# Performance work log

Measured on AMD Instinct MI355X. Metric: run time of the kernel, lower is better.

## Reference

```python
import jax, jax.numpy as jnp
import numpy as np


def setup_inputs() -> dict:
    key = jax.random.key(0)
    k1, k2 = jax.random.split(key)
    B, N, Fin, Fout, K = 4, 4096, 64, 64, 20
    x = jax.random.normal(k1, (B, N, Fin), dtype=jnp.float32)
    # nn.Linear(2*Fin, Fout): weight [Fout, 2*Fin], bias [Fout]
    W = jax.random.normal(k2, (Fout, 2 * Fin), dtype=jnp.float32) * (1.0 / np.sqrt(2 * Fin))
    b = jnp.zeros((Fout,), dtype=jnp.float32)
    return {"x": x, "W": W, "b": b, "k": K}


def _edge_features(x, k):
    # x: [B, N, F] -> edge features [B, N, k, 2F]
    # pairwise squared distance: ||xi||^2 - 2 xi.xj + ||xj||^2
    xs = jnp.sum(x * x, axis=2, keepdims=True)            # [B, N, 1]
    dist = xs - 2.0 * jnp.einsum('bnf,bmf->bnm', x, x) + jnp.swapaxes(xs, 1, 2)  # [B, N, N]
    idx = jnp.argsort(dist, axis=2)[:, :, 1:k + 1]        # skip self -> [B, N, k]
    # gather neighbor features per batch (vectorized index_select)
    neighbors = jax.vmap(lambda xb, ib: xb[ib])(x, idx)   # [B, N, k, F]
    central = jnp.broadcast_to(x[:, :, None, :], neighbors.shape)
    return jnp.concatenate([central, neighbors - central], axis=3)  # [B, N, k, 2F]


def reference(x, W, b, k):
    ee = _edge_features(x, k)                 # [B, N, k, 2F]
    h = jnp.einsum('bnkc,oc->bnko', ee, W) + b  # Linear(2F -> Fout)
    return jnp.max(h, axis=2)                 # max over k neighbors -> [B, N, Fout]
```

## Files before the change

kernel.cpp:

```cpp
#include <hip/hip_runtime.h>
#include <float.h>


constexpr int Bb = 4, Nn = 4096, Ff = 64, Kk = 20;

typedef __attribute__((ext_vector_type(8))) short bf16x8;
typedef __attribute__((ext_vector_type(16))) float f32x16;

__device__ inline unsigned int bf16rn(float f) {
  unsigned int u = __float_as_uint(f);
  return (u + 0x7fffu + ((u >> 16) & 1u)) >> 16;
}

constexpr int RT1 = 16;

__global__ __launch_bounds__(256) void uv_kernel2(
    const float* __restrict__ x, const float* __restrict__ W,
    const float* __restrict__ bvec, float* __restrict__ u,
    float* __restrict__ v, float* __restrict__ sq,
    unsigned short* __restrict__ xhi, unsigned short* __restrict__ xlo) {
  __shared__ __align__(16) float4 Ws[64 * 33];
  __shared__ __align__(16) float4 xs[RT1 * 16];
  const int t = threadIdx.x, l = t & 63, w = t >> 6;
  const int bn0 = blockIdx.x * RT1;
  #pragma unroll
  for (int i = 0; i < 8; i++) {
    int f = t + 256 * i;
    Ws[(f >> 5) * 33 + (f & 31)] = ((const float4*)W)[f];
  }
  xs[t] = ((const float4*)x)[bn0 * 16 + t];
  __syncthreads();
  #pragma unroll
  for (int i = 0; i < 4; i++) {
    int idx = t + 256 * i;
    int nloc = idx >> 6;
    int k = idx & 63;
    float val = ((const float*)xs)[idx];
    unsigned int hb = bf16rn(val);
    float fhi = __uint_as_float(hb << 16);
    unsigned int lb = bf16rn(val - fhi);
    int ng = bn0 + nloc;
    size_t flat = ((size_t)(ng >> 5) << 11) + ((size_t)(k >> 4) << 9) +
                  ((size_t)((k >> 3) & 1) << 8) + ((size_t)(ng & 31) << 3) +
                  (size_t)(k & 7);
    xhi[flat] = (unsigned short)hb;
    xlo[flat] = (unsigned short)lb;
  }
  #pragma unroll
  for (int i = 0; i < 4; i++) {
    int r = 4 * w + i;
    float val = ((const float*)&xs[r * 16])[l];
    float s = val * val;
    #pragma unroll
    for (int d = 32; d; d >>= 1) s += __shfl_xor(s, d, 64);
    if (l == 0) sq[bn0 + r] = s;
  }
  const int o = l;
  float ua[4] = {0.f, 0.f, 0.f, 0.f}, va[4] = {0.f, 0.f, 0.f, 0.f};
  #pragma unroll
  for (int c = 0; c < 16; c++) {
    float4 w1 = Ws[o * 33 + c];
    float4 w2 = Ws[o * 33 + 16 + c];
    float4 wd;
    wd.x = w1.x - w2.x; wd.y = w1.y - w2.y;
    wd.z = w1.z - w2.z; wd.w = w1.w - w2.w;
    #pragma unroll
    for (int i = 0; i < 4; i++) {
      float4 xv = xs[(4 * w + i) * 16 + c];
      ua[i] += xv.x * wd.x + xv.y * wd.y + xv.z * wd.z + xv.w * wd.w;
      va[i] += xv.x * w2.x + xv.y * w2.y + xv.z * w2.z + xv.w * w2.w;
    }
  }
  float bo = bvec[o];
  #pragma unroll
  for (int i = 0; i < 4; i++) {
    size_t row = (size_t)(bn0 + 4 * w + i);
    u[row * 64 + o] = ua[i] + bo;
    v[row * 64 + o] = va[i];
  }
}


__global__ __launch_bounds__(256) void key_mfma_kernel(
    const unsigned short* __restrict__ xhi,
    const unsigned short* __restrict__ xlo, const float* __restrict__ sq,
    unsigned short* __restrict__ keys) {
  const int t = threadIdx.x, l = t & 63, w = t >> 6;
  const int blk = blockIdx.x;
  const int b = blk >> 8;
  const int r = blk & 255;
  const int n_base = (r >> 1) * 32;
  const int m0w = (r & 1) * 2048 + w * 512;
  const int col = l & 31, half = l >> 5;

  const unsigned short* xhb = xhi + (size_t)b * Nn * Ff;
  const unsigned short* xlb = xlo + (size_t)b * Nn * Ff;
  const float* sqb = sq + b * Nn;

  bf16x8 Ahi[4], Alo[4];
  #pragma unroll
  for (int ks = 0; ks < 4; ks++) {
    size_t off = ((size_t)((n_base >> 5) * 4 + ks) << 9) + ((size_t)l << 3);
    Ahi[ks] = *(const bf16x8*)(xhb + off);
    Alo[ks] = *(const bf16x8*)(xlb + off);
  }
  float sqn_r[16];
  #pragma unroll
  for (int e = 0; e < 16; e++) {
    int row = (e & 3) + 8 * (e >> 2) + 4 * half;
    sqn_r[e] = sqb[n_base + row];
  }

  for (int j = 0; j < 16; ++j) {
    const int m0 = m0w + 32 * j;
    const int mblk = m0 >> 5;
    bf16x8 Bhi[4], Blo[4];
    #pragma unroll
    for (int ks = 0; ks < 4; ks++) {
      size_t off = ((size_t)(mblk * 4 + ks) << 9) + ((size_t)l << 3);
      Bhi[ks] = *(const bf16x8*)(xhb + off);
      Blo[ks] = *(const bf16x8*)(xlb + off);
    }
    f32x16 acc = {0.f, 0.f, 0.f, 0.f, 0.f, 0.f, 0.f, 0.f,
                  0.f, 0.f, 0.f, 0.f, 0.f, 0.f, 0.f, 0.f};
    #pragma unroll
    for (int ks = 0; ks < 4; ks++) {
      acc = __builtin_amdgcn_mfma_f32_32x32x16_bf16(Ahi[ks], Bhi[ks], acc, 0, 0, 0);
      acc = __builtin_amdgcn_mfma_f32_32x32x16_bf16(Ahi[ks], Blo[ks], acc, 0, 0, 0);
      acc = __builtin_amdgcn_mfma_f32_32x32x16_bf16(Alo[ks], Bhi[ks], acc, 0, 0, 0);
    }
    const int m = m0 + col;
    const float sm = sqb[m];
    #pragma unroll
    for (int e = 0; e < 16; e++) {
      int row = (e & 3) + 8 * (e >> 2) + 4 * half;
      int n = n_base + row;
      float d = fmaxf(sqn_r[e] + sm - 2.0f * acc[e], 0.f);
      unsigned int key = __float_as_uint(d) >> 15;
      if (m == n) key = 0xFFFFu;
      keys[((size_t)(b * Nn + n) << 12) + m] = (unsigned short)key;
    }
  }
}

__global__ __launch_bounds__(256) void select_kernel(
    const float* __restrict__ x, const unsigned short* __restrict__ keys,
    const float* __restrict__ u, const float* __restrict__ v,
    float* __restrict__ out) {
  __shared__ int candS[4 * 64];
  __shared__ int ccntS[4];
  const int t = threadIdx.x, l = t & 63, w = t >> 6;
  const int row = blockIdx.x * 4 + w;
  const int rowu = __builtin_amdgcn_readfirstlane(row);
  const int b = rowu >> 12, n = rowu & (Nn - 1);
  const uint4* kr = (const uint4*)(keys + (size_t)rowu * Nn);
  uint4 kv[8];
  #pragma unroll
  for (int j = 0; j < 8; j++) kv[j] = kr[j * 64 + l];

  auto countLE = [&](int mid) -> int {
    int c = 0;
    #pragma unroll
    for (int j = 0; j < 8; j++) {
      unsigned int a0 = kv[j].x, a1 = kv[j].y, a2 = kv[j].z, a3 = kv[j].w;
      c += ((int)(a0 & 0xffffu) <= mid) + ((int)(a0 >> 16) <= mid);
      c += ((int)(a1 & 0xffffu) <= mid) + ((int)(a1 >> 16) <= mid);
      c += ((int)(a2 & 0xffffu) <= mid) + ((int)(a2 >> 16) <= mid);
      c += ((int)(a3 & 0xffffu) <= mid) + ((int)(a3 >> 16) <= mid);
    }
    #pragma unroll
    for (int d2 = 1; d2 < 64; d2 <<= 1) c += __shfl_xor(c, d2, 64);
    return c;
  };

  unsigned int mn = 0xffffffffu;
  #pragma unroll
  for (int j = 0; j < 8; j++) {
    unsigned int a0 = kv[j].x, a1 = kv[j].y, a2 = kv[j].z, a3 = kv[j].w;
    mn = min(mn, min(min(a0 & 0xffffu, a0 >> 16), min(a1 & 0xffffu, a1 >> 16)));
    mn = min(mn, min(min(a2 & 0xffffu, a2 >> 16), min(a3 & 0xffffu, a3 >> 16)));
  }
  #pragma unroll
  for (int d2 = 1; d2 < 64; d2 <<= 1)
    mn = min(mn, (unsigned int)__shfl_xor((int)mn, d2, 64));

  int lo = (int)mn - 1;
  int hi = (int)mn + 64;
  if (hi > 65534) hi = 65534;
  int c = countLE(hi);
  int step = 128;
  while (c < Kk && hi < 65534) {
    lo = hi;
    hi += step;
    if (hi > 65534) hi = 65534;
    step <<= 1;
    c = countLE(hi);
  }
  while (c > 44 && hi - lo > 1) {
    int mid = (lo + hi) >> 1;
    int cm = countLE(mid);
    if (cm >= Kk) { hi = mid; c = cm; } else { lo = mid; }
  }
  const int hc = hi + 1;

  if (l == 0) ccntS[w] = 0;
  #pragma unroll
  for (int j = 0; j < 8; j++) {
    unsigned int a[4] = {kv[j].x, kv[j].y, kv[j].z, kv[j].w};
    #pragma unroll
    for (int e = 0; e < 4; e++) {
      int base = ((j * 64 + l) * 4 + e) * 2;
      if ((int)(a[e] & 0xffffu) <= hc) {
        int slot = atomicAdd(&ccntS[w], 1);
        if (slot < 64) candS[w * 64 + slot] = base;
      }
      if ((int)(a[e] >> 16) <= hc) {
        int slot = atomicAdd(&ccntS[w], 1);
        if (slot < 64) candS[w * 64 + slot] = base + 1;
      }
    }
  }
  int C = ccntS[w];
  if (C > 64) C = 64;

  const float4* xb4 = (const float4*)(x + (size_t)b * Nn * Ff);
  unsigned long long key64 = ~0ULL;
  if (l < C) {
    int mI = candS[w * 64 + l];
    const float4* xmf = xb4 + (size_t)mI * 16;
    float ds = 0.f;
    #pragma unroll
    for (int cc = 0; cc < 16; cc++) {
      float4 a = xb4[(size_t)n * 16 + cc];
      float4 bb = xmf[cc];
      float dx = a.x - bb.x, dy = a.y - bb.y, dz = a.z - bb.z, dw2 = a.w - bb.w;
      ds += dx * dx + dy * dy + dz * dz + dw2 * dw2;
    }
    if (mI == n) ds = FLT_MAX;
    key64 = ((unsigned long long)__float_as_uint(ds) << 32) | (unsigned int)mI;
  }

  float vmax = -FLT_MAX;
  const float* vb = v + (size_t)b * Nn * Ff;
  #pragma unroll
  for (int it = 0; it < Kk; ++it) {
    unsigned long long kmin = key64;
    #pragma unroll
    for (int d2 = 1; d2 < 64; d2 <<= 1) {
      unsigned long long o =
          (unsigned long long)__shfl_xor((long long)kmin, d2, 64);
      kmin = (o < kmin) ? o : kmin;
    }
    int mI = (int)(kmin & 0xffffffffu) & (Nn - 1);
    vmax = fmaxf(vmax, vb[(size_t)mI * 64 + l]);
    if (key64 == kmin) key64 = ~0ULL;
  }
  const size_t oidx = (size_t)rowu * 64 + l;
  out[oidx] = u[oidx] + vmax;
}

constexpr int RTF = 4;
constexpr int MTF = 64;
constexpr int TPADF = 17;
constexpr int CCAPF = 64;

__global__ __launch_bounds__(256) void knn_kernel(
    const float* __restrict__ x, const float* __restrict__ sq,
    const float* __restrict__ u, const float* __restrict__ v,
    float* __restrict__ out) {
  __shared__ __align__(16) float4 tileS[MTF * TPADF];
  __shared__ __align__(16) unsigned short keysS[RTF * Nn];
  __shared__ int candS[RTF * CCAPF];
  __shared__ int ccntS[RTF];
  const int t = threadIdx.x;
  const int l = t & 63, w = t >> 6;
  const int q = l & 15, g = l >> 4;
  const int bn0 = blockIdx.x * RTF;
  const int b = bn0 >> 12;
  const int n0 = bn0 & (Nn - 1);
  const float4* xb4 = (const float4*)(x + (size_t)b * Nn * Ff);
  const float* sqb = sq + b * Nn;
  if (t < RTF) ccntS[t] = 0;
  float4 xnq[RTF][4];
  #pragma unroll
  for (int r = 0; r < RTF; r++)
    #pragma unroll
    for (int c = 0; c < 4; c++) xnq[r][c] = xb4[(n0 + r) * 16 + 4 * g + c];
  const float sn = sqb[n0 + g];
  const int selfm = n0 + g;
  for (int T = 0; T < Nn / MTF; ++T) {
    __syncthreads();
    #pragma unroll
    for (int i = 0; i < 4; i++) {
      int f = t + 256 * i;
      tileS[(f >> 4) * TPADF + (f & 15)] = xb4[T * 1024 + f];
    }
    __syncthreads();
    const int mrow = 16 * w + q;
    const float4* xmp = &tileS[mrow * TPADF + 4 * g];
    float4 xm0 = xmp[0], xm1 = xmp[1], xm2 = xmp[2], xm3 = xmp[3];
    float dot[RTF];
    #pragma unroll
    for (int r = 0; r < RTF; r++) {
      float4 a0 = xnq[r][0], a1 = xnq[r][1], a2 = xnq[r][2], a3 = xnq[r][3];
      dot[r] = a0.x * xm0.x + a0.y * xm0.y + a0.z * xm0.z + a0.w * xm0.w +
               a1.x * xm1.x + a1.y * xm1.y + a1.z * xm1.z + a1.w * xm1.w +
               a2.x * xm2.x + a2.y * xm2.y + a2.z * xm2.z + a2.w * xm2.w +
               a3.x * xm3.x + a3.y * xm3.y + a3.z * xm3.z + a3.w * xm3.w;
    }
    #pragma unroll
    for (int r = 0; r < RTF; r++) {
      dot[r] += __shfl_xor(dot[r], 16, 64);
      dot[r] += __shfl_xor(dot[r], 32, 64);
    }
    float dg = (g == 0) ? dot[0] : (g == 1) ? dot[1] : (g == 2) ? dot[2] : dot[3];
    int m = T * MTF + mrow;
    float d = fmaxf(fmaf(-2.f, dg, sqb[m] + sn), 0.f);
    unsigned int key = __float_as_uint(d) >> 15;
    if (m == selfm) key = 0xFFFFu;
    keysS[g * Nn + m] = (unsigned short)key;
  }
  __syncthreads();
  const unsigned int* kp = (const unsigned int*)&keysS[w * Nn];
  int lo = -1, hi = 65535, cntHi = Nn;
  while (cntHi > 48 && hi - lo > 1) {
    int mid = (lo + hi) >> 1;
    unsigned int midu = (unsigned int)mid;
    int c = 0;
    #pragma unroll
    for (int cc = 0; cc < 8; ++cc) {
      int rc = (cc + l) & 7;
      uint4 k4 = *(const uint4*)(kp + l * 32 + rc * 4);
      c += ((k4.x & 0xffffu) <= midu) + ((k4.x >> 16) <= midu);
      c += ((k4.y & 0xffffu) <= midu) + ((k4.y >> 16) <= midu);
      c += ((k4.z & 0xffffu) <= midu) + ((k4.z >> 16) <= midu);
      c += ((k4.w & 0xffffu) <= midu) + ((k4.w >> 16) <= midu);
    }
    #pragma unroll
    for (int d2 = 1; d2 < 64; d2 <<= 1) c += __shfl_xor(c, d2, 64);
    if (c >= Kk) { hi = mid; cntHi = c; } else { lo = mid; }
  }
  {
    unsigned int hu = (unsigned int)hi;
    #pragma unroll
    for (int cc = 0; cc < 8; ++cc) {
      int rc = (cc + l) & 7;
      uint4 k4 = *(const uint4*)(kp + l * 32 + rc * 4);
      unsigned int ks[4] = {k4.x, k4.y, k4.z, k4.w};
      #pragma unroll
      for (int uu = 0; uu < 4; ++uu) {
        #pragma unroll
        for (int hh = 0; hh < 2; ++hh) {
          unsigned int kvv = hh ? (ks[uu] >> 16) : (ks[uu] & 0xffffu);
          if (kvv <= hu) {
            int slot = atomicAdd(&ccntS[w], 1);
            if (slot < CCAPF) candS[w * CCAPF + slot] = l * 64 + (rc * 4 + uu) * 2 + hh;
          }
        }
      }
    }
  }
  __syncthreads();
  const int n = n0 + w;
  const int C = min(cntHi, CCAPF);
  unsigned long long key64 = ~0ULL;
  if (l < C) {
    int mI = candS[w * CCAPF + l];
    const float4* xmf = xb4 + mI * 16;
    float ds = 0.f;
    #pragma unroll
    for (int c = 0; c < 16; c++) {
      float4 a = xb4[n * 16 + c];
      float4 bb = xmf[c];
      float dx = a.x - bb.x, dy = a.y - bb.y, dz = a.z - bb.z, dw2 = a.w - bb.w;
      ds += dx * dx + dy * dy + dz * dz + dw2 * dw2;
    }
    key64 = ((unsigned long long)__float_as_uint(ds) << 32) | (unsigned int)mI;
  }
  float vmax = -FLT_MAX;
  const float* vb = v + (size_t)b * Nn * Ff;
  #pragma unroll
  for (int it = 0; it < Kk; ++it) {
    unsigned long long kmin = key64;
    #pragma unroll
    for (int d2 = 1; d2 < 64; d2 <<= 1) {
      unsigned long long o =
          (unsigned long long)__shfl_xor((long long)kmin, d2, 64);
      kmin = (o < kmin) ? o : kmin;
    }
    int mI = (int)(kmin & 0xffffffffu) & (Nn - 1);
    vmax = fmaxf(vmax, vb[(size_t)mI * 64 + l]);
    if (key64 == kmin) key64 = ~0ULL;
  }
  const size_t oidx = (size_t)(bn0 + w) * 64 + l;
  out[oidx] = u[oidx] + vmax;
}

extern "C" void kernel_launch(void* const* d_in, const int* in_sizes, int n_in,
                              void* d_out, int out_size, void* d_ws,
                              size_t ws_size, hipStream_t stream) {
  const float* x = (const float*)d_in[0];
  const float* W = (const float*)d_in[1];
  const float* bvec = (const float*)d_in[2];
  float* u = (float*)d_ws;
  float* v = u + (size_t)Bb * Nn * Ff;
  float* sq = v + (size_t)Bb * Nn * Ff;
  unsigned short* xhi = (unsigned short*)(sq + (size_t)Bb * Nn);
  unsigned short* xlo = xhi + (size_t)Bb * Nn * Ff;
  unsigned short* keys = xlo + (size_t)Bb * Nn * Ff;
  float* out = (float*)d_out;
  const size_t need = (size_t)Bb * Nn * Ff * 4 * 2 + (size_t)Bb * Nn * 4 +
                      (size_t)Bb * Nn * Ff * 2 * 2 + (size_t)Bb * Nn * Nn * 2;

  uv_kernel2<<<Bb * Nn / RT1, 256, 0, stream>>>(x, W, bvec, u, v, sq, xhi, xlo);
  if (ws_size >= need) {
    key_mfma_kernel<<<Bb * Nn / 16, 256, 0, stream>>>(xhi, xlo, sq, keys);
    select_kernel<<<Bb * Nn / 4, 256, 0, stream>>>(x, keys, u, v, out);
  } else {
    knn_kernel<<<Bb * Nn / RTF, 256, 0, stream>>>(x, sq, u, v, out);
  }
}
```

Measured before the change: 178.2 us.

## Pair-reduce distance keys with min before storing to halve key traffic

The MFMA key kernel now takes the min over pairs of columns 32 apart and writes one 16-bit key per pair, packed two to a 32-bit word. This halves the key matrix that is written and then read back. The select kernel scans half as many keys and recomputes exact distances for both columns of each candidate pair, merging them in the top-k loop. The threshold gets slightly more slack to stay correct, at the cost of more exact-distance work per candidate. It also adds a launch_bounds occupancy hint on the key kernel.

```diff
diff --git a/kernel.cpp b/kernel.cpp
--- a/kernel.cpp
+++ b/kernel.cpp
@@ -81,10 +81,10 @@
 }
 
 
-__global__ __launch_bounds__(256) void key_mfma_kernel(
+__global__ __launch_bounds__(256, 4) void key_mfma_kernel(
     const unsigned short* __restrict__ xhi,
     const unsigned short* __restrict__ xlo, const float* __restrict__ sq,
-    unsigned short* __restrict__ keys) {
+    unsigned int* __restrict__ keys) {
   const int t = threadIdx.x, l = t & 63, w = t >> 6;
   const int blk = blockIdx.x;
   const int b = blk >> 8;
@@ -105,46 +105,59 @@
     Alo[ks] = *(const bf16x8*)(xlb + off);
   }
   float sqn_r[16];
+  int nrow_r[16];
   #pragma unroll
   for (int e = 0; e < 16; e++) {
     int row = (e & 3) + 8 * (e >> 2) + 4 * half;
-    sqn_r[e] = sqb[n_base + row];
-  }
-
-  for (int j = 0; j < 16; ++j) {
-    const int m0 = m0w + 32 * j;
-    const int mblk = m0 >> 5;
-    bf16x8 Bhi[4], Blo[4];
-    #pragma unroll
-    for (int ks = 0; ks < 4; ks++) {
-      size_t off = ((size_t)(mblk * 4 + ks) << 9) + ((size_t)l << 3);
-      Bhi[ks] = *(const bf16x8*)(xhb + off);
-      Blo[ks] = *(const bf16x8*)(xlb + off);
-    }
-    f32x16 acc = {0.f, 0.f, 0.f, 0.f, 0.f, 0.f, 0.f, 0.f,
-                  0.f, 0.f, 0.f, 0.f, 0.f, 0.f, 0.f, 0.f};
-    #pragma unroll
-    for (int ks = 0; ks < 4; ks++) {
-      acc = __builtin_amdgcn_mfma_f32_32x32x16_bf16(Ahi[ks], Bhi[ks], acc, 0, 0, 0);
-      acc = __builtin_amdgcn_mfma_f32_32x32x16_bf16(Ahi[ks], Blo[ks], acc, 0, 0, 0);
-      acc = __builtin_amdgcn_mfma_f32_32x32x16_bf16(Alo[ks], Bhi[ks], acc, 0, 0, 0);
-    }
-    const int m = m0 + col;
-    const float sm = sqb[m];
+    nrow_r[e] = n_base + row;
+    sqn_r[e] = sqb[nrow_r[e]];
+  }
+
+  for (int jq = 0; jq < 4; ++jq) {
+    const int base = m0w + 128 * jq;
+    unsigned int pmin[2][16];
+    #pragma unroll
+    for (int q = 0; q < 4; q++) {
+      const int m0 = base + 32 * q;
+      const int mblk = m0 >> 5;
+      bf16x8 Bhi[4], Blo[4];
+      #pragma unroll
+      for (int ks = 0; ks < 4; ks++) {
+        size_t off = ((size_t)(mblk * 4 + ks) << 9) + ((size_t)l << 3);
+        Bhi[ks] = *(const bf16x8*)(xhb + off);
+        Blo[ks] = *(const bf16x8*)(xlb + off);
+      }
+      f32x16 acc = {0.f, 0.f, 0.f, 0.f, 0.f, 0.f, 0.f, 0.f,
+                    0.f, 0.f, 0.f, 0.f, 0.f, 0.f, 0.f, 0.f};
+      #pragma unroll
+      for (int ks = 0; ks < 4; ks++) {
+        acc = __builtin_amdgcn_mfma_f32_32x32x16_bf16(Ahi[ks], Bhi[ks], acc, 0, 0, 0);
+        acc = __builtin_amdgcn_mfma_f32_32x32x16_bf16(Ahi[ks], Blo[ks], acc, 0, 0, 0);
+        acc = __builtin_amdgcn_mfma_f32_32x32x16_bf16(Alo[ks], Bhi[ks], acc, 0, 0, 0);
+      }
+      const int m = m0 + col;
+      const float sm = sqb[m];
+      #pragma unroll
+      for (int e = 0; e < 16; e++) {
+        float d = fmaxf(sqn_r[e] + sm - 2.0f * acc[e], 0.f);
+        unsigned int key = __float_as_uint(d) >> 15;
+        if (m == nrow_r[e]) key = 0xFFFFu;
+        if (q & 1)
+          pmin[q >> 1][e] = min(pmin[q >> 1][e], key);
+        else
+          pmin[q >> 1][e] = key;
+      }
+    }
     #pragma unroll
     for (int e = 0; e < 16; e++) {
-      int row = (e & 3) + 8 * (e >> 2) + 4 * half;
-      int n = n_base + row;
-      float d = fmaxf(sqn_r[e] + sm - 2.0f * acc[e], 0.f);
-      unsigned int key = __float_as_uint(d) >> 15;
-      if (m == n) key = 0xFFFFu;
-      keys[((size_t)(b * Nn + n) << 12) + m] = (unsigned short)key;
+      unsigned int pk = pmin[0][e] | (pmin[1][e] << 16);
+      keys[(size_t)(b * Nn + nrow_r[e]) * 1024 + (base >> 7) * 32 + col] = pk;
     }
   }
 }
 
 __global__ __launch_bounds__(256) void select_kernel(
-    const float* __restrict__ x, const unsigned short* __restrict__ keys,
+    const float* __restrict__ x, const unsigned int* __restrict__ keys,
     const float* __restrict__ u, const float* __restrict__ v,
     float* __restrict__ out) {
   __shared__ int candS[4 * 64];
@@ -153,15 +166,15 @@
   const int row = blockIdx.x * 4 + w;
   const int rowu = __builtin_amdgcn_readfirstlane(row);
   const int b = rowu >> 12, n = rowu & (Nn - 1);
-  const uint4* kr = (const uint4*)(keys + (size_t)rowu * Nn);
-  uint4 kv[8];
-  #pragma unroll
-  for (int j = 0; j < 8; j++) kv[j] = kr[j * 64 + l];
+  const uint4* kr = (const uint4*)(keys + (size_t)rowu * 1024);
+  uint4 kv[4];
+  #pragma unroll
+  for (int j = 0; j < 4; j++) kv[j] = kr[j * 64 + l];
 
   auto countLE = [&](int mid) -> int {
     int c = 0;
     #pragma unroll
-    for (int j = 0; j < 8; j++) {
+    for (int j = 0; j < 4; j++) {
       unsigned int a0 = kv[j].x, a1 = kv[j].y, a2 = kv[j].z, a3 = kv[j].w;
       c += ((int)(a0 & 0xffffu) <= mid) + ((int)(a0 >> 16) <= mid);
       c += ((int)(a1 & 0xffffu) <= mid) + ((int)(a1 >> 16) <= mid);
@@ -175,7 +188,7 @@
 
   unsigned int mn = 0xffffffffu;
   #pragma unroll
-  for (int j = 0; j < 8; j++) {
+  for (int j = 0; j < 4; j++) {
     unsigned int a0 = kv[j].x, a1 = kv[j].y, a2 = kv[j].z, a3 = kv[j].w;
     mn = min(mn, min(min(a0 & 0xffffu, a0 >> 16), min(a1 & 0xffffu, a1 >> 16)));
     mn = min(mn, min(min(a2 & 0xffffu, a2 >> 16), min(a3 & 0xffffu, a3 >> 16)));
@@ -186,13 +199,13 @@
 
   int lo = (int)mn - 1;
   int hi = (int)mn + 64;
-  if (hi > 65534) hi = 65534;
+  if (hi > 65533) hi = 65533;
   int c = countLE(hi);
   int step = 128;
-  while (c < Kk && hi < 65534) {
+  while (c < Kk && hi < 65533) {
     lo = hi;
     hi += step;
-    if (hi > 65534) hi = 65534;
+    if (hi > 65533) hi = 65533;
     step <<= 1;
     c = countLE(hi);
   }
@@ -201,22 +214,22 @@
     int cm = countLE(mid);
     if (cm >= Kk) { hi = mid; c = cm; } else { lo = mid; }
   }
-  const int hc = hi + 1;
+  const int hc = hi + 2;
 
   if (l == 0) ccntS[w] = 0;
   #pragma unroll
-  for (int j = 0; j < 8; j++) {
+  for (int j = 0; j < 4; j++) {
     unsigned int a[4] = {kv[j].x, kv[j].y, kv[j].z, kv[j].w};
     #pragma unroll
     for (int e = 0; e < 4; e++) {
-      int base = ((j * 64 + l) * 4 + e) * 2;
+      int dwi = (j * 64 + l) * 4 + e;
       if ((int)(a[e] & 0xffffu) <= hc) {
         int slot = atomicAdd(&ccntS[w], 1);
-        if (slot < 64) candS[w * 64 + slot] = base;
+        if (slot < 64) candS[w * 64 + slot] = 2 * dwi;
       }
       if ((int)(a[e] >> 16) <= hc) {
         int slot = atomicAdd(&ccntS[w], 1);
-        if (slot < 64) candS[w * 64 + slot] = base + 1;
+        if (slot < 64) candS[w * 64 + slot] = 2 * dwi + 1;
       }
     }
   }
@@ -224,27 +237,38 @@
   if (C > 64) C = 64;
 
   const float4* xb4 = (const float4*)(x + (size_t)b * Nn * Ff);
-  unsigned long long key64 = ~0ULL;
+  unsigned long long ka = ~0ULL, kb = ~0ULL;
   if (l < C) {
-    int mI = candS[w * 64 + l];
-    const float4* xmf = xb4 + (size_t)mI * 16;
-    float ds = 0.f;
+    int i = candS[w * 64 + l];
+    int dwi = i >> 1, sel = i & 1;
+    int chunk = dwi >> 5, colp = dwi & 31;
+    int m1 = chunk * 128 + sel * 64 + colp;
+    int m2 = m1 + 32;
+    const float4* xm1 = xb4 + (size_t)m1 * 16;
+    const float4* xm2 = xb4 + (size_t)m2 * 16;
+    float ds1 = 0.f, ds2 = 0.f;
     #pragma unroll
     for (int cc = 0; cc < 16; cc++) {
       float4 a = xb4[(size_t)n * 16 + cc];
-      float4 bb = xmf[cc];
-      float dx = a.x - bb.x, dy = a.y - bb.y, dz = a.z - bb.z, dw2 = a.w - bb.w;
-      ds += dx * dx + dy * dy + dz * dz + dw2 * dw2;
-    }
-    if (mI == n) ds = FLT_MAX;
-    key64 = ((unsigned long long)__float_as_uint(ds) << 32) | (unsigned int)mI;
+      float4 b1 = xm1[cc];
+      float4 b2 = xm2[cc];
+      float dx = a.x - b1.x, dy = a.y - b1.y, dz = a.z - b1.z, dw2 = a.w - b1.w;
+      ds1 += dx * dx + dy * dy + dz * dz + dw2 * dw2;
+      dx = a.x - b2.x; dy = a.y - b2.y; dz = a.z - b2.z; dw2 = a.w - b2.w;
+      ds2 += dx * dx + dy * dy + dz * dz + dw2 * dw2;
+    }
+    if (m1 == n) ds1 = FLT_MAX;
+    if (m2 == n) ds2 = FLT_MAX;
+    ka = ((unsigned long long)__float_as_uint(ds1) << 32) | (unsigned int)m1;
+    kb = ((unsigned long long)__float_as_uint(ds2) << 32) | (unsigned int)m2;
   }
 
   float vmax = -FLT_MAX;
   const float* vb = v + (size_t)b * Nn * Ff;
   #pragma unroll
   for (int it = 0; it < Kk; ++it) {
-    unsigned long long kmin = key64;
+    unsigned long long loc = (ka < kb) ? ka : kb;
+    unsigned long long kmin = loc;
     #pragma unroll
     for (int d2 = 1; d2 < 64; d2 <<= 1) {
       unsigned long long o =
@@ -253,7 +277,8 @@
     }
     int mI = (int)(kmin & 0xffffffffu) & (Nn - 1);
     vmax = fmaxf(vmax, vb[(size_t)mI * 64 + l]);
-    if (key64 == kmin) key64 = ~0ULL;
+    if (ka == kmin) ka = ~0ULL;
+    else if (kb == kmin) kb = ~0ULL;
   }
   const size_t oidx = (size_t)rowu * 64 + l;
   out[oidx] = u[oidx] + vmax;
@@ -407,10 +432,11 @@
   float* sq = v + (size_t)Bb * Nn * Ff;
   unsigned short* xhi = (unsigned short*)(sq + (size_t)Bb * Nn);
   unsigned short* xlo = xhi + (size_t)Bb * Nn * Ff;
-  unsigned short* keys = xlo + (size_t)Bb * Nn * Ff;
+  unsigned int* keys = (unsigned int*)(xlo + (size_t)Bb * Nn * Ff);
   float* out = (float*)d_out;
   const size_t need = (size_t)Bb * Nn * Ff * 4 * 2 + (size_t)Bb * Nn * 4 +
-                      (size_t)Bb * Nn * Ff * 2 * 2 + (size_t)Bb * Nn * Nn * 2;
+                      (size_t)Bb * Nn * Ff * 2 * 2 +
+                      (size_t)Bb * Nn * 1024 * 4;
 
   uv_kernel2<<<Bb * Nn / RT1, 256, 0, stream>>>(x, W, bvec, u, v, sq, xhi, xlo);
   if (ws_size >= need) {
```

Result: slower. 222.4 us (+24.8%).
